# Performance work log

Hardware: AMD Instinct MI355X
Metric: run time of the kernel (lower is better)

The kernel has to match this reference:

```python
import jax, jax.numpy as jnp
import numpy as np

B, L, K, D = 1024, 128, 16, 512
NUM_FEATURES, NUM_LABELS, NUM_NEG = 100000, 131072, 2048
EPS = 0.1
C = 2.0 + EPS  # spherical kernel constant


def safe_log(x, eps=1e-08):
    return jnp.log(jnp.maximum(x, eps))


def safe_normalize(x, axis=-1, eps=0.0001):
    norm = jnp.linalg.norm(x, axis=axis, keepdims=True)
    return x / jnp.maximum(norm, eps)


def setup_inputs() -> dict:
    key = jax.random.key(0)
    k0, k1, k2, k3, k4 = jax.random.split(key, 5)
    indices = jax.random.randint(k0, (B, L), 0, NUM_FEATURES)
    mask = jnp.ones((B, L), jnp.float32)
    labels = jax.random.randint(k1, (B, K), 0, NUM_LABELS)
    label_mask = jnp.ones((B, K), jnp.float32)
    neg_indices = jax.random.randint(k2, (NUM_NEG,), 0, NUM_LABELS)
    embed_table = jax.random.normal(k3, (NUM_FEATURES, D), jnp.float32) * 0.02
    W_kernel = jax.random.normal(k4, (D, NUM_LABELS), jnp.float32) * 0.02  # nnx.Linear kernel (in, out)
    return {"indices": indices, "mask": mask, "labels": labels,
            "label_mask": label_mask, "neg_indices": neg_indices,
            "embed_table": embed_table, "W_kernel": W_kernel}


def reference(indices, mask, labels, label_mask, neg_indices, embed_table, W_kernel):
    # MeanEmbedding encoder
    embeds = embed_table[indices]                                  # [B, L, D]
    sum_embeds = jnp.sum(embeds * mask[:, :, None], axis=1)        # [B, D]
    enc = sum_embeds / jnp.maximum(jnp.sum(mask, axis=1, keepdims=True), 1.0)
    query = safe_normalize(enc, axis=-1)                           # [B, D]
    W = safe_normalize(W_kernel.T, axis=-1)                        # [NUM_LABELS, D]

    safe_labels = jnp.maximum(labels, 0)
    all_indices = jnp.concatenate([safe_labels.reshape(-1), neg_indices])  # [B*K + NN]
    W_subset = W[all_indices]                                      # [B*K+NN, D]

    # spherical Yat kernel: dot^2 / max(C - 2*dot, eps)
    dot = jnp.clip(query @ W_subset.T, -0.999, 0.999)              # [B, B*K+NN]
    scores = dot ** 2 / jnp.maximum(C - 2.0 * dot, EPS)

    idx_offsets = jnp.arange(B)[:, None] * K + jnp.arange(K)[None, :]
    pos_scores = jnp.take_along_axis(scores, idx_offsets, axis=1)  # [B, K]
    neg_scores = scores[:, B * K:]                                 # [B, NN]
    all_scores = jnp.concatenate([pos_scores, neg_scores], axis=1) + 1e-08
    log_Z = jax.scipy.special.logsumexp(safe_log(all_scores), axis=1)
    log_probs = safe_log(pos_scores + 1e-08) - log_Z[:, None]
    return -jnp.sum(log_probs * label_mask) / (jnp.sum(label_mask) + 1e-06)
```

## Files before the change

kernel.cpp:

```cpp
#include <hip/hip_runtime.h>
#include <hip/hip_bf16.h>

#define BDIM 1024
#define LDIM 128
#define KDIM 16
#define DDIM 512
#define NLAB 131072
#define NNEG 2048
#define NPOS (BDIM * KDIM)
#define NSUB (NPOS + NNEG)
#define EPSV 0.1f
#define CV 2.1f
#define NBUCK 512
#define GT_BLOCKS (NBUCK * 8)

typedef __attribute__((ext_vector_type(8))) short s8v;
typedef __attribute__((ext_vector_type(4))) float f4v;
typedef __attribute__((ext_vector_type(4))) float fv4;

static __device__ __forceinline__ unsigned short f2bf(float x) {
    union { float f; unsigned u; } v; v.f = x;
    unsigned r = v.u + 0x7FFF + ((v.u >> 16) & 1);
    return (unsigned short)(r >> 16);
}
static __device__ __forceinline__ float bf2f(unsigned short h) {
    return __uint_as_float((unsigned)h << 16);
}

__global__ __launch_bounds__(256) void init_kernel(int* __restrict__ cnt,
                                                   float* __restrict__ norms2,
                                                   float* __restrict__ Zrow,
                                                   float* __restrict__ accum,
                                                   int* __restrict__ ticket) {
    int j = blockIdx.x * 256 + threadIdx.x;
    if (j < NSUB) norms2[j] = 0.f;
    if (j < NBUCK) cnt[j] = 0;
    if (j < BDIM) Zrow[j] = 0.f;
    if (j < 2) accum[j] = 0.f;
    if (j == 0) *ticket = 0;
}

__global__ __launch_bounds__(256) void count_kernel(const int* __restrict__ labels,
                                                    const int* __restrict__ negs,
                                                    int* __restrict__ all_idx,
                                                    int* __restrict__ cnt) {
    int j = blockIdx.x * 256 + threadIdx.x;
    if (j >= NSUB) return;
    int v = (j < NPOS) ? max(labels[j], 0) : negs[j - NPOS];
    all_idx[j] = v;
    atomicAdd(&cnt[v >> 8], 1);
}

__global__ __launch_bounds__(256) void scan_kernel(const int* __restrict__ cnt,
                                                   int* __restrict__ offs) {
    int t = threadIdx.x;
    int a0 = cnt[2 * t], a1 = cnt[2 * t + 1];
    int chunk = a0 + a1;
    int ts = chunk;
    int lane = t & 63, wid = t >> 6;
    #pragma unroll
    for (int off = 1; off < 64; off <<= 1) {
        int v = __shfl_up(ts, off, 64);
        if (lane >= off) ts += v;
    }
    __shared__ int wsum[4];
    if (lane == 63) wsum[wid] = ts;
    __syncthreads();
    int woff = 0;
    for (int w = 0; w < wid; ++w) woff += wsum[w];
    int incl = woff + ts;
    int excl = incl - chunk;
    offs[2 * t]     = excl;
    offs[2 * t + 1] = excl + a0;
}

__global__ __launch_bounds__(256) void place_kernel(const int* __restrict__ all_idx,
                                                    int* __restrict__ offs,
                                                    int* __restrict__ srt_v,
                                                    int* __restrict__ rank) {
    int j = blockIdx.x * 256 + threadIdx.x;
    if (j >= NSUB) return;
    int v = all_idx[j];
    int r = atomicAdd(&offs[v >> 8], 1);
    srt_v[r] = v;
    rank[j] = r;
}

__global__ __launch_bounds__(256) void main1_kernel(const float* __restrict__ Wk,
                                                    const int* __restrict__ srt_v,
                                                    const int* __restrict__ offs_end,
                                                    const int* __restrict__ cnt,
                                                    unsigned short* __restrict__ WT,
                                                    float* __restrict__ norms2,
                                                    const int* __restrict__ indices,
                                                    const float* __restrict__ mask,
                                                    const float* __restrict__ embed,
                                                    float* __restrict__ query,
                                                    unsigned short* __restrict__ qbf) {
    __shared__ __align__(16) unsigned short tile[256][65];
    int t = threadIdx.x;
    int w = t >> 6, l = t & 63;

    if (blockIdx.x < BDIM) {
        int*   sidx  = (int*)&tile[0][0];
        float* smask = (float*)&tile[16][0];
        float* red   = (float*)&tile[32][0];
        float* snorm = (float*)&tile[33][0];
        int b = blockIdx.x;
        if (t < LDIM) {
            sidx[t]  = indices[b * LDIM + t];
            smask[t] = mask[b * LDIM + t];
        }
        __syncthreads();
        float ax = 0.f, ay = 0.f, msum = 0.f;
        #pragma unroll 2
        for (int ll = 0; ll < LDIM; ll += 4) {
            int   i0 = sidx[ll],   i1 = sidx[ll + 1],  i2 = sidx[ll + 2],  i3 = sidx[ll + 3];
            float m0 = smask[ll],  m1 = smask[ll + 1], m2 = smask[ll + 2], m3 = smask[ll + 3];
            float2 r0 = *(const float2*)&embed[(size_t)i0 * DDIM + t * 2];
            float2 r1 = *(const float2*)&embed[(size_t)i1 * DDIM + t * 2];
            float2 r2 = *(const float2*)&embed[(size_t)i2 * DDIM + t * 2];
            float2 r3 = *(const float2*)&embed[(size_t)i3 * DDIM + t * 2];
            msum += m0 + m1 + m2 + m3;
            ax += m0 * r0.x + m1 * r1.x + m2 * r2.x + m3 * r3.x;
            ay += m0 * r0.y + m1 * r1.y + m2 * r2.y + m3 * r3.y;
        }
        float denom = fmaxf(msum, 1.0f);
        ax /= denom; ay /= denom;
        float ss = ax * ax + ay * ay;
        #pragma unroll
        for (int off = 32; off > 0; off >>= 1) ss += __shfl_down(ss, off, 64);
        if (l == 0) red[w] = ss;
        __syncthreads();
        if (t == 0) snorm[0] = sqrtf(red[0] + red[1] + red[2] + red[3]);
        __syncthreads();
        float inv = 1.f / fmaxf(snorm[0], 1e-4f);
        float2 o = { ax * inv, ay * inv };
        *(float2*)&query[(size_t)b * DDIM + t * 2] = o;
        ushort2 ob = { f2bf(o.x), f2bf(o.y) };
        *(ushort2*)&qbf[(size_t)b * DDIM + t * 2] = ob;
    } else {
        int bt = blockIdx.x - BDIM;
        int g  = bt >> 3;
        int dt = bt & 7;
        int d0 = dt * 64;
        #pragma unroll
        for (int i = 0; i < 16; ++i) {
            int dl = w * 16 + i;
            fv4 v = __builtin_nontemporal_load(
                (const fv4*)&Wk[(size_t)(d0 + dl) * NLAB + g * 256 + l * 4]);
            tile[l * 4 + 0][dl] = f2bf(v.x);
            tile[l * 4 + 1][dl] = f2bf(v.y);
            tile[l * 4 + 2][dl] = f2bf(v.z);
            tile[l * 4 + 3][dl] = f2bf(v.w);
        }
        __syncthreads();
        int rend = offs_end[g];
        int rbeg = rend - cnt[g];
        for (int r = rbeg + w; r < rend; r += 4) {
            int v = srt_v[r];
            int col = v - g * 256;
            unsigned short h = tile[col][l];
            WT[(size_t)r * DDIM + d0 + l] = h;
            float f = bf2f(h);
            float ss = f * f;
            ss += __shfl_xor(ss, 1, 64);  ss += __shfl_xor(ss, 2, 64);
            ss += __shfl_xor(ss, 4, 64);  ss += __shfl_xor(ss, 8, 64);
            ss += __shfl_xor(ss, 16, 64); ss += __shfl_xor(ss, 32, 64);
            if (l == 0) atomicAdd(&norms2[r], ss);
        }
    }
}

static __device__ __forceinline__ float score_of(float acc, float nn) {
    float dot = acc / nn;
    dot = fminf(fmaxf(dot, -0.999f), 0.999f);
    return dot * dot / fmaxf(CV - 2.f * dot, EPSV);
}

__global__ __launch_bounds__(256) void main2_kernel(const unsigned short* __restrict__ qbf,
                                                    const float* __restrict__ query,
                                                    const unsigned short* __restrict__ WT,
                                                    const int* __restrict__ rank,
                                                    const float* __restrict__ norms2,
                                                    float* __restrict__ pos_scores,
                                                    float* __restrict__ Zrow) {
    int t = threadIdx.x;
    int w = t >> 6, l = t & 63;
    if (blockIdx.x < (BDIM / 64) * (NNEG / 64)) {
        __shared__ float rowsum[64];
        int bx = blockIdx.x;
        int mt = bx & 15, nt = bx >> 4;
        int wm = w >> 1, wn = w & 1;
        int lr = l & 15, lg = l >> 4;
        int m0 = mt * 64 + wm * 32;
        int n0 = nt * 64 + wn * 32;
        if (t < 64) rowsum[t] = 0.f;
        __syncthreads();

        int rB0 = rank[NPOS + n0 + lr];
        int rB1 = rank[NPOS + n0 + 16 + lr];
        const unsigned short* a0p = qbf + (size_t)(m0 + lr) * DDIM + lg * 8;
        const unsigned short* a1p = qbf + (size_t)(m0 + 16 + lr) * DDIM + lg * 8;
        const unsigned short* b0p = WT + (size_t)rB0 * DDIM + lg * 8;
        const unsigned short* b1p = WT + (size_t)rB1 * DDIM + lg * 8;

        f4v acc00 = {0.f, 0.f, 0.f, 0.f}, acc01 = acc00, acc10 = acc00, acc11 = acc00;
        #pragma unroll
        for (int k0 = 0; k0 < DDIM; k0 += 32) {
            s8v a0 = *(const s8v*)(a0p + k0);
            s8v a1 = *(const s8v*)(a1p + k0);
            s8v b0 = *(const s8v*)(b0p + k0);
            s8v b1 = *(const s8v*)(b1p + k0);
            acc00 = __builtin_amdgcn_mfma_f32_16x16x32_bf16(a0, b0, acc00, 0, 0, 0);
            acc01 = __builtin_amdgcn_mfma_f32_16x16x32_bf16(a0, b1, acc01, 0, 0, 0);
            acc10 = __builtin_amdgcn_mfma_f32_16x16x32_bf16(a1, b0, acc10, 0, 0, 0);
            acc11 = __builtin_amdgcn_mfma_f32_16x16x32_bf16(a1, b1, acc11, 0, 0, 0);
        }

        float nn0 = fmaxf(sqrtf(norms2[rB0]), 1e-4f);
        float nn1 = fmaxf(sqrtf(norms2[rB1]), 1e-4f);
        float s[8];
        #pragma unroll
        for (int i = 0; i < 4; ++i) {
            s[i]     = score_of(acc00[i], nn0) + score_of(acc01[i], nn1);
            s[4 + i] = score_of(acc10[i], nn0) + score_of(acc11[i], nn1);
        }
        #pragma unroll
        for (int i = 0; i < 8; ++i) {
            s[i] += __shfl_xor(s[i], 1, 64);
            s[i] += __shfl_xor(s[i], 2, 64);
            s[i] += __shfl_xor(s[i], 4, 64);
            s[i] += __shfl_xor(s[i], 8, 64);
        }
        if (lr == 0) {
            #pragma unroll
            for (int i = 0; i < 4; ++i) {
                atomicAdd(&rowsum[wm * 32 + lg * 4 + i], s[i]);
                atomicAdd(&rowsum[wm * 32 + 16 + lg * 4 + i], s[4 + i]);
            }
        }
        __syncthreads();
        if (t < 64) atomicAdd(&Zrow[mt * 64 + t], rowsum[t]);
    } else {
        int px = blockIdx.x - (BDIM / 64) * (NNEG / 64);
        int b = px * 4 + w;
        int j = b * KDIM + (l & 15);
        int r = rank[j];
        int g = l >> 4;
        const unsigned short* wrow = WT + (size_t)r * DDIM + g * 128;
        const float* qrow = query + (size_t)b * DDIM + g * 128;
        float acc = 0.f;
        #pragma unroll
        for (int kk = 0; kk < 128; kk += 8) {
            ushort4 w0 = *(const ushort4*)&wrow[kk];
            ushort4 w1 = *(const ushort4*)&wrow[kk + 4];
            float4 q0 = *(const float4*)&qrow[kk];
            float4 q1 = *(const float4*)&qrow[kk + 4];
            acc += bf2f(w0.x) * q0.x + bf2f(w0.y) * q0.y + bf2f(w0.z) * q0.z + bf2f(w0.w) * q0.w
                 + bf2f(w1.x) * q1.x + bf2f(w1.y) * q1.y + bf2f(w1.z) * q1.z + bf2f(w1.w) * q1.w;
        }
        acc += __shfl_xor(acc, 16, 64);
        acc += __shfl_xor(acc, 32, 64);
        if (l < 16) {
            float nrm = fmaxf(sqrtf(norms2[r]), 1e-4f);
            float dot = fminf(fmaxf(acc / nrm, -0.999f), 0.999f);
            float sc = dot * dot / fmaxf(CV - 2.f * dot, EPSV);
            pos_scores[j] = sc;
            float s = sc;
            s += __shfl_xor(s, 1, 64); s += __shfl_xor(s, 2, 64);
            s += __shfl_xor(s, 4, 64); s += __shfl_xor(s, 8, 64);
            if (l == 0) atomicAdd(&Zrow[b], s);
        }
    }
}

__global__ __launch_bounds__(256) void finalize_kernel(const float* __restrict__ pos_scores,
                                                       const float* __restrict__ label_mask,
                                                       const float* __restrict__ Zrow,
                                                       float* __restrict__ accum,
                                                       int* __restrict__ ticket,
                                                       float* __restrict__ out) {
    int j = blockIdx.x * 256 + threadIdx.x;
    int b = j >> 4;
    float lm = label_mask[j];
    float logZ = logf(Zrow[b] + (float)(KDIM + NNEG) * 1e-8f);
    float v = lm * (logf(pos_scores[j] + 1e-8f) - logZ);
    #pragma unroll
    for (int off = 32; off > 0; off >>= 1) {
        v  += __shfl_down(v, off, 64);
        lm += __shfl_down(lm, off, 64);
    }
    __shared__ float rv[4], rl[4];
    int wid = threadIdx.x >> 6, lane = threadIdx.x & 63;
    if (lane == 0) { rv[wid] = v; rl[wid] = lm; }
    __syncthreads();
    if (threadIdx.x == 0) {
        atomicAdd(&accum[0], rv[0] + rv[1] + rv[2] + rv[3]);
        atomicAdd(&accum[1], rl[0] + rl[1] + rl[2] + rl[3]);
        __threadfence();
        int old = atomicAdd(ticket, 1);
        if (old == (int)gridDim.x - 1) {
            float a = atomicAdd(&accum[0], 0.f);
            float m = atomicAdd(&accum[1], 0.f);
            out[0] = -a / (m + 1e-6f);
        }
    }
}

extern "C" void kernel_launch(void* const* d_in, const int* in_sizes, int n_in,
                              void* d_out, int out_size, void* d_ws, size_t ws_size,
                              hipStream_t stream) {
    const int*   indices    = (const int*)  d_in[0];
    const float* mask       = (const float*)d_in[1];
    const int*   labels     = (const int*)  d_in[2];
    const float* label_mask = (const float*)d_in[3];
    const int*   negs       = (const int*)  d_in[4];
    const float* embed      = (const float*)d_in[5];
    const float* Wk         = (const float*)d_in[6];
    float* out = (float*)d_out;

    unsigned short* WT  = (unsigned short*)d_ws;
    float* query      = (float*)(WT + (size_t)NSUB * DDIM);
    unsigned short* qbf = (unsigned short*)(query + (size_t)BDIM * DDIM);
    int*   all_idx    = (int*)(qbf + (size_t)BDIM * DDIM);
    int*   srt_v      = all_idx + NSUB;
    int*   rank       = srt_v + NSUB;
    float* norms2     = (float*)(rank + NSUB);
    float* pos_scores = norms2 + NSUB;
    float* Zrow       = pos_scores + NPOS;
    float* accum      = Zrow + BDIM;
    int*   ticket     = (int*)(accum + 2);
    int*   cnt        = ticket + 1;
    int*   offs       = cnt + NBUCK;

    init_kernel<<<NSUB / 256, 256, 0, stream>>>(cnt, norms2, Zrow, accum, ticket);
    count_kernel<<<NSUB / 256, 256, 0, stream>>>(labels, negs, all_idx, cnt);
    scan_kernel<<<1, 256, 0, stream>>>(cnt, offs);
    place_kernel<<<NSUB / 256, 256, 0, stream>>>(all_idx, offs, srt_v, rank);
    main1_kernel<<<BDIM + GT_BLOCKS, 256, 0, stream>>>(Wk, srt_v, offs, cnt, WT, norms2,
                                                       indices, mask, embed, query, qbf);
    main2_kernel<<<(BDIM / 64) * (NNEG / 64) + NPOS / 64, 256, 0, stream>>>(
        qbf, query, WT, rank, norms2, pos_scores, Zrow);
    finalize_kernel<<<NPOS / 256, 256, 0, stream>>>(pos_scores, label_mask, Zrow,
                                                    accum, ticket, out);
}
```

Measured before the change: 148.7 us.

## Fuse bucket sort into single-block kernel and widen query gather to float4

Result: slower. 153.6 us (+3.3%).

```diff
diff --git a/kernel.cpp b/kernel.cpp
--- a/kernel.cpp
+++ b/kernel.cpp
@@ -12,11 +12,13 @@
 #define EPSV 0.1f
 #define CV 2.1f
 #define NBUCK 512
+#define QBLK (BDIM / 2)
 #define GT_BLOCKS (NBUCK * 8)
 
 typedef __attribute__((ext_vector_type(8))) short s8v;
 typedef __attribute__((ext_vector_type(4))) float f4v;
 typedef __attribute__((ext_vector_type(4))) float fv4;
+typedef __attribute__((ext_vector_type(4))) unsigned short us4;
 
 static __device__ __forceinline__ unsigned short f2bf(float x) {
     union { float f; unsigned u; } v; v.f = x;
@@ -27,63 +29,55 @@
     return __uint_as_float((unsigned)h << 16);
 }
 
-__global__ __launch_bounds__(256) void init_kernel(int* __restrict__ cnt,
-                                                   float* __restrict__ norms2,
+__global__ __launch_bounds__(256) void init_kernel(float* __restrict__ norms2,
                                                    float* __restrict__ Zrow,
                                                    float* __restrict__ accum,
                                                    int* __restrict__ ticket) {
     int j = blockIdx.x * 256 + threadIdx.x;
     if (j < NSUB) norms2[j] = 0.f;
-    if (j < NBUCK) cnt[j] = 0;
     if (j < BDIM) Zrow[j] = 0.f;
     if (j < 2) accum[j] = 0.f;
     if (j == 0) *ticket = 0;
 }
 
-__global__ __launch_bounds__(256) void count_kernel(const int* __restrict__ labels,
-                                                    const int* __restrict__ negs,
-                                                    int* __restrict__ all_idx,
-                                                    int* __restrict__ cnt) {
-    int j = blockIdx.x * 256 + threadIdx.x;
-    if (j >= NSUB) return;
-    int v = (j < NPOS) ? max(labels[j], 0) : negs[j - NPOS];
-    all_idx[j] = v;
-    atomicAdd(&cnt[v >> 8], 1);
-}
-
-__global__ __launch_bounds__(256) void scan_kernel(const int* __restrict__ cnt,
-                                                   int* __restrict__ offs) {
+__global__ __launch_bounds__(1024) void sortall_kernel(const int* __restrict__ labels,
+                                                       const int* __restrict__ negs,
+                                                       int* __restrict__ offs_end,
+                                                       int* __restrict__ cntg,
+                                                       int* __restrict__ srt_v,
+                                                       int* __restrict__ rank) {
+    __shared__ int sc[NBUCK];
     int t = threadIdx.x;
-    int a0 = cnt[2 * t], a1 = cnt[2 * t + 1];
-    int chunk = a0 + a1;
-    int ts = chunk;
-    int lane = t & 63, wid = t >> 6;
+    if (t < NBUCK) sc[t] = 0;
+    __syncthreads();
+    int vs[NSUB / 1024];
     #pragma unroll
-    for (int off = 1; off < 64; off <<= 1) {
-        int v = __shfl_up(ts, off, 64);
-        if (lane >= off) ts += v;
-    }
-    __shared__ int wsum[4];
-    if (lane == 63) wsum[wid] = ts;
-    __syncthreads();
-    int woff = 0;
-    for (int w = 0; w < wid; ++w) woff += wsum[w];
-    int incl = woff + ts;
-    int excl = incl - chunk;
-    offs[2 * t]     = excl;
-    offs[2 * t + 1] = excl + a0;
-}
-
-__global__ __launch_bounds__(256) void place_kernel(const int* __restrict__ all_idx,
-                                                    int* __restrict__ offs,
-                                                    int* __restrict__ srt_v,
-                                                    int* __restrict__ rank) {
-    int j = blockIdx.x * 256 + threadIdx.x;
-    if (j >= NSUB) return;
-    int v = all_idx[j];
-    int r = atomicAdd(&offs[v >> 8], 1);
-    srt_v[r] = v;
-    rank[j] = r;
+    for (int k = 0; k < NSUB / 1024; ++k) {
+        int j = k * 1024 + t;
+        int v = (j < NPOS) ? max(labels[j], 0) : negs[j - NPOS];
+        vs[k] = v;
+        atomicAdd(&sc[v >> 8], 1);
+    }
+    __syncthreads();
+    int c = (t < NBUCK) ? sc[t] : 0;
+    for (int off = 1; off < NBUCK; off <<= 1) {
+        int v2 = (t < NBUCK && t >= off) ? sc[t - off] : 0;
+        __syncthreads();
+        if (t < NBUCK) sc[t] += v2;
+        __syncthreads();
+    }
+    if (t < NBUCK) { cntg[t] = c; sc[t] -= c; }
+    __syncthreads();
+    #pragma unroll
+    for (int k = 0; k < NSUB / 1024; ++k) {
+        int j = k * 1024 + t;
+        int v = vs[k];
+        int r = atomicAdd(&sc[v >> 8], 1);
+        srt_v[r] = v;
+        rank[j] = r;
+    }
+    __syncthreads();
+    if (t < NBUCK) offs_end[t] = sc[t];
 }
 
 __global__ __launch_bounds__(256) void main1_kernel(const float* __restrict__ Wk,
@@ -101,46 +95,46 @@
     int t = threadIdx.x;
     int w = t >> 6, l = t & 63;
 
-    if (blockIdx.x < BDIM) {
+    if (blockIdx.x < QBLK) {
         int*   sidx  = (int*)&tile[0][0];
-        float* smask = (float*)&tile[16][0];
-        float* red   = (float*)&tile[32][0];
-        float* snorm = (float*)&tile[33][0];
-        int b = blockIdx.x;
-        if (t < LDIM) {
-            sidx[t]  = indices[b * LDIM + t];
-            smask[t] = mask[b * LDIM + t];
-        }
-        __syncthreads();
-        float ax = 0.f, ay = 0.f, msum = 0.f;
-        #pragma unroll 2
-        for (int ll = 0; ll < LDIM; ll += 4) {
-            int   i0 = sidx[ll],   i1 = sidx[ll + 1],  i2 = sidx[ll + 2],  i3 = sidx[ll + 3];
-            float m0 = smask[ll],  m1 = smask[ll + 1], m2 = smask[ll + 2], m3 = smask[ll + 3];
-            float2 r0 = *(const float2*)&embed[(size_t)i0 * DDIM + t * 2];
-            float2 r1 = *(const float2*)&embed[(size_t)i1 * DDIM + t * 2];
-            float2 r2 = *(const float2*)&embed[(size_t)i2 * DDIM + t * 2];
-            float2 r3 = *(const float2*)&embed[(size_t)i3 * DDIM + t * 2];
-            msum += m0 + m1 + m2 + m3;
-            ax += m0 * r0.x + m1 * r1.x + m2 * r2.x + m3 * r3.x;
-            ay += m0 * r0.y + m1 * r1.y + m2 * r2.y + m3 * r3.y;
+        float* smask = (float*)&tile[8][0];
+        float* red   = (float*)&tile[17][0];
+        float* snorm = (float*)&tile[18][0];
+        int half = t >> 7;
+        int tc = t & 127;
+        int b = blockIdx.x * 2 + half;
+        sidx[half * 128 + tc]  = indices[b * LDIM + tc];
+        smask[half * 128 + tc] = mask[b * LDIM + tc];
+        __syncthreads();
+        float msum = 0.f;
+        for (int i = 0; i < LDIM; ++i) msum += smask[half * 128 + i];
+        fv4 acc = {0.f, 0.f, 0.f, 0.f};
+        #pragma unroll 4
+        for (int ll = 0; ll < LDIM; ++ll) {
+            int   idx = sidx[half * 128 + ll];
+            float m   = smask[half * 128 + ll];
+            fv4 v = *(const fv4*)&embed[(size_t)idx * DDIM + tc * 4];
+            acc += v * m;
         }
         float denom = fmaxf(msum, 1.0f);
-        ax /= denom; ay /= denom;
-        float ss = ax * ax + ay * ay;
-        #pragma unroll
-        for (int off = 32; off > 0; off >>= 1) ss += __shfl_down(ss, off, 64);
+        acc /= denom;
+        float ss = acc[0] * acc[0] + acc[1] * acc[1] + acc[2] * acc[2] + acc[3] * acc[3];
+        #pragma unroll
+        for (int off = 32; off > 0; off >>= 1) ss += __shfl_xor(ss, off, 64);
         if (l == 0) red[w] = ss;
         __syncthreads();
-        if (t == 0) snorm[0] = sqrtf(red[0] + red[1] + red[2] + red[3]);
-        __syncthreads();
-        float inv = 1.f / fmaxf(snorm[0], 1e-4f);
-        float2 o = { ax * inv, ay * inv };
-        *(float2*)&query[(size_t)b * DDIM + t * 2] = o;
-        ushort2 ob = { f2bf(o.x), f2bf(o.y) };
-        *(ushort2*)&qbf[(size_t)b * DDIM + t * 2] = ob;
+        if (t == 0) {
+            snorm[0] = sqrtf(red[0] + red[1]);
+            snorm[1] = sqrtf(red[2] + red[3]);
+        }
+        __syncthreads();
+        float inv = 1.f / fmaxf(snorm[half], 1e-4f);
+        acc *= inv;
+        __builtin_nontemporal_store(acc, (fv4*)&query[(size_t)b * DDIM + tc * 4]);
+        us4 ob = { f2bf(acc[0]), f2bf(acc[1]), f2bf(acc[2]), f2bf(acc[3]) };
+        __builtin_nontemporal_store(ob, (us4*)&qbf[(size_t)b * DDIM + tc * 4]);
     } else {
-        int bt = blockIdx.x - BDIM;
+        int bt = blockIdx.x - QBLK;
         int g  = bt >> 3;
         int dt = bt & 7;
         int d0 = dt * 64;
@@ -149,10 +143,10 @@
             int dl = w * 16 + i;
             fv4 v = __builtin_nontemporal_load(
                 (const fv4*)&Wk[(size_t)(d0 + dl) * NLAB + g * 256 + l * 4]);
-            tile[l * 4 + 0][dl] = f2bf(v.x);
-            tile[l * 4 + 1][dl] = f2bf(v.y);
-            tile[l * 4 + 2][dl] = f2bf(v.z);
-            tile[l * 4 + 3][dl] = f2bf(v.w);
+            tile[l * 4 + 0][dl] = f2bf(v[0]);
+            tile[l * 4 + 1][dl] = f2bf(v[1]);
+            tile[l * 4 + 2][dl] = f2bf(v[2]);
+            tile[l * 4 + 3][dl] = f2bf(v[3]);
         }
         __syncthreads();
         int rend = offs_end[g];
@@ -161,7 +155,7 @@
             int v = srt_v[r];
             int col = v - g * 256;
             unsigned short h = tile[col][l];
-            WT[(size_t)r * DDIM + d0 + l] = h;
+            __builtin_nontemporal_store(h, &WT[(size_t)r * DDIM + d0 + l]);
             float f = bf2f(h);
             float ss = f * f;
             ss += __shfl_xor(ss, 1, 64);  ss += __shfl_xor(ss, 2, 64);
@@ -323,22 +317,19 @@
     unsigned short* WT  = (unsigned short*)d_ws;
     float* query      = (float*)(WT + (size_t)NSUB * DDIM);
     unsigned short* qbf = (unsigned short*)(query + (size_t)BDIM * DDIM);
-    int*   all_idx    = (int*)(qbf + (size_t)BDIM * DDIM);
-    int*   srt_v      = all_idx + NSUB;
+    int*   srt_v      = (int*)(qbf + (size_t)BDIM * DDIM);
     int*   rank       = srt_v + NSUB;
     float* norms2     = (float*)(rank + NSUB);
     float* pos_scores = norms2 + NSUB;
     float* Zrow       = pos_scores + NPOS;
     float* accum      = Zrow + BDIM;
     int*   ticket     = (int*)(accum + 2);
-    int*   cnt        = ticket + 1;
-    int*   offs       = cnt + NBUCK;
-
-    init_kernel<<<NSUB / 256, 256, 0, stream>>>(cnt, norms2, Zrow, accum, ticket);
-    count_kernel<<<NSUB / 256, 256, 0, stream>>>(labels, negs, all_idx, cnt);
-    scan_kernel<<<1, 256, 0, stream>>>(cnt, offs);
-    place_kernel<<<NSUB / 256, 256, 0, stream>>>(all_idx, offs, srt_v, rank);
-    main1_kernel<<<BDIM + GT_BLOCKS, 256, 0, stream>>>(Wk, srt_v, offs, cnt, WT, norms2,
+    int*   cntg       = ticket + 1;
+    int*   offs_end   = cntg + NBUCK;
+
+    init_kernel<<<NSUB / 256, 256, 0, stream>>>(norms2, Zrow, accum, ticket);
+    sortall_kernel<<<1, 1024, 0, stream>>>(labels, negs, offs_end, cntg, srt_v, rank);
+    main1_kernel<<<QBLK + GT_BLOCKS, 256, 0, stream>>>(Wk, srt_v, offs_end, cntg, WT, norms2,
                                                        indices, mask, embed, query, qbf);
     main2_kernel<<<(BDIM / 64) * (NNEG / 64) + NPOS / 64, 256, 0, stream>>>(
         qbf, query, WT, rank, norms2, pos_scores, Zrow);
```
